# Performance work log

Measured on AMD Instinct MI355X. Metric: run time of the kernel, lower is better.

The kernel has to match this reference:

```python
import jax, jax.numpy as jnp
import numpy as np

N_NODES = 100_000
N_EDGES = 1_600_000
HIDDEN = 256
N_LAYERS = 5
N_GRAPHS = 256
NUM_ATOM_TYPE = 120
NUM_CHIRALITY = 3
NUM_BOND_TYPE = 6
NUM_BOND_DIR = 3


def setup_inputs() -> dict:
    key = jax.random.key(0)
    ks = jax.random.split(key, 16)
    x = jax.random.randint(ks[0], (N_NODES, 2), 0, 3)
    edge_index = jax.random.randint(ks[1], (2, N_EDGES), 0, N_NODES)
    edge_attr = jax.random.randint(ks[2], (N_EDGES, 2), 0, 3)
    batch = jnp.sort(jax.random.randint(ks[3], (N_NODES,), 0, N_GRAPHS))
    # embedding tables (xavier-uniform-ish scale)
    def emb(k, n, d):
        a = np.sqrt(6.0 / (n + d))
        return jax.random.uniform(k, (n, d), jnp.float32, -a, a)
    xe1 = emb(ks[4], NUM_ATOM_TYPE, HIDDEN)
    xe2 = emb(ks[5], NUM_CHIRALITY, HIDDEN)
    ee1 = emb(ks[6], NUM_BOND_TYPE, HIDDEN)
    ee2 = emb(ks[7], NUM_BOND_DIR, HIDDEN)
    s = 1.0 / np.sqrt(HIDDEN)
    W1 = jax.random.uniform(ks[8], (N_LAYERS, HIDDEN, HIDDEN), jnp.float32, -s, s)
    b1 = jax.random.uniform(ks[9], (N_LAYERS, HIDDEN), jnp.float32, -s, s)
    W2 = jax.random.uniform(ks[10], (N_LAYERS, HIDDEN, HIDDEN), jnp.float32, -s, s)
    b2 = jax.random.uniform(ks[11], (N_LAYERS, HIDDEN), jnp.float32, -s, s)
    return {"x": x, "edge_index": edge_index, "edge_attr": edge_attr, "batch": batch,
            "xe1": xe1, "xe2": xe2, "ee1": ee1, "ee2": ee2,
            "W1": W1, "b1": b1, "W2": W2, "b2": b2}


def reference(x, edge_index, edge_attr, batch, xe1, xe2, ee1, ee2, W1, b1, W2, b2):
    # node / edge input embeddings (sum of two lookups)
    z = xe1[x[:, 0]] + xe2[x[:, 1]]                      # [N, H]
    e = ee1[edge_attr[:, 0]] + ee2[edge_attr[:, 1]]      # [E, H]
    src, dst = edge_index[0], edge_index[1]
    for l in range(N_LAYERS):
        # GINEConv: nn((1+eps)*x_i + sum_j relu(x_j + e_ij)), eps = 0
        msg = jax.nn.relu(z[src] + e)                    # [E, H]
        agg = jax.ops.segment_sum(msg, dst, num_segments=N_NODES)
        h = z + agg                                      # (1+0)*x + aggr
        h = jax.nn.relu(h @ W1[l] + b1[l]) @ W2[l] + b2[l]
        z = jax.nn.relu(h)                               # outer relu in GIN.forward
    # global mean pool over graphs
    sums = jax.ops.segment_sum(z, batch, num_segments=N_GRAPHS)      # [G, H]
    cnts = jax.ops.segment_sum(jnp.ones((z.shape[0], 1), z.dtype), batch, num_segments=N_GRAPHS)
    g = sums / jnp.maximum(cnts, 1.0)
    # dropout p=0.0 -> identity
    return (z, g)
```

## Files before the change

kernel.cpp:

```cpp
#include <hip/hip_runtime.h>
#include <hip/hip_bf16.h>

#define HID 256
#define NCODES 18
#define SCAN_CHUNK 2048
#define LROW 264

typedef _Float16 h8_t __attribute__((ext_vector_type(8)));
typedef _Float16 h4_t __attribute__((ext_vector_type(4)));
typedef float f4_t __attribute__((ext_vector_type(4)));

__global__ void etab_kernel(const float* __restrict__ ee1, const float* __restrict__ ee2,
                            _Float16* __restrict__ etab) {
    int t = blockIdx.x;
    int c = threadIdx.x;
    etab[t * HID + c] = (_Float16)(ee1[(t / 3) * HID + c] + ee2[(t % 3) * HID + c]);
}

__global__ __launch_bounds__(256) void embed_kernel(const int* __restrict__ x,
                                                    const float* __restrict__ xe1,
                                                    const float* __restrict__ xe2,
                                                    _Float16* __restrict__ zh, int N) {
    int node = blockIdx.x * 4 + (threadIdx.x >> 6);
    int lane = threadIdx.x & 63;
    if (node >= N) return;
    int a0 = x[node * 2 + 0];
    int a1 = x[node * 2 + 1];
    const float4 u = *(const float4*)(xe1 + (size_t)a0 * HID + lane * 4);
    const float4 v = *(const float4*)(xe2 + (size_t)a1 * HID + lane * 4);
    h4_t r;
    r.x = (_Float16)(u.x + v.x); r.y = (_Float16)(u.y + v.y);
    r.z = (_Float16)(u.z + v.z); r.w = (_Float16)(u.w + v.w);
    *(h4_t*)(zh + (size_t)node * HID + lane * 4) = r;
}

__global__ __launch_bounds__(256) void prep_w(const float* __restrict__ W,
                                              _Float16* __restrict__ Wt) {
    __shared__ float t[32][33];
    int m = blockIdx.z;
    int tx = threadIdx.x & 31, ty = threadIdx.x >> 5;
    const float* Wm = W + (size_t)m * HID * HID;
    _Float16* Wtm = Wt + (size_t)m * HID * HID;
    int k0 = blockIdx.x * 32, n0 = blockIdx.y * 32;
#pragma unroll
    for (int j = 0; j < 4; ++j) { int r = ty + j * 8; t[r][tx] = Wm[(k0 + r) * HID + n0 + tx]; }
    __syncthreads();
#pragma unroll
    for (int j = 0; j < 4; ++j) { int r = ty + j * 8; Wtm[(size_t)(n0 + r) * HID + k0 + tx] = (_Float16)t[tx][r]; }
}

__global__ void hist_kernel(const int* __restrict__ ei, int E, int* __restrict__ deg) {
    int i = blockIdx.x * 256 + threadIdx.x;
    if (i < E) atomicAdd(&deg[ei[E + i]], 1);
}

__global__ __launch_bounds__(256) void scan_partial(const int* __restrict__ deg, int n,
                                                    int* __restrict__ psum) {
    __shared__ int red[256];
    int base = blockIdx.x * SCAN_CHUNK;
    int s = 0;
    for (int i = threadIdx.x; i < SCAN_CHUNK; i += 256) {
        int idx = base + i;
        if (idx < n) s += deg[idx];
    }
    red[threadIdx.x] = s;
    __syncthreads();
    for (int off = 128; off > 0; off >>= 1) {
        if (threadIdx.x < off) red[threadIdx.x] += red[threadIdx.x + off];
        __syncthreads();
    }
    if (threadIdx.x == 0) psum[blockIdx.x] = red[0];
}

__global__ void scan_sums(int* psum, int nchunks) {
    if (blockIdx.x == 0 && threadIdx.x == 0) {
        int acc = 0;
        for (int i = 0; i < nchunks; i++) { int v = psum[i]; psum[i] = acc; acc += v; }
    }
}

__global__ __launch_bounds__(256) void scan_apply(const int* __restrict__ deg, int n,
                                                  const int* __restrict__ psum,
                                                  int* __restrict__ row_start,
                                                  int* __restrict__ cursor, int E) {
    __shared__ int tmp[256];
    int tid = threadIdx.x;
    int base = blockIdx.x * SCAN_CHUNK;
    int tb = base + tid * 8;
    int loc[8];
    int s = 0;
    for (int j = 0; j < 8; j++) {
        loc[j] = s;
        int idx = tb + j;
        if (idx < n) s += deg[idx];
    }
    tmp[tid] = s;
    __syncthreads();
    for (int off = 1; off < 256; off <<= 1) {
        int v = 0;
        if (tid >= off) v = tmp[tid - off];
        __syncthreads();
        if (tid >= off) tmp[tid] += v;
        __syncthreads();
    }
    int excl = tmp[tid] - s + psum[blockIdx.x];
    for (int j = 0; j < 8; j++) {
        int idx = tb + j;
        if (idx < n) {
            int v = excl + loc[j];
            row_start[idx] = v;
            cursor[idx] = v;
        }
    }
    if (blockIdx.x == 0 && tid == 0) row_start[n] = E;
}

__global__ void fill_kernel(const int* __restrict__ ei, const int* __restrict__ ea, int E,
                            int* __restrict__ cursor, unsigned* __restrict__ csr) {
    int i = blockIdx.x * 256 + threadIdx.x;
    if (i >= E) return;
    int dst = ei[E + i];
    int src = ei[i];
    int code = ea[i * 2] * 3 + ea[i * 2 + 1];
    int p = atomicAdd(&cursor[dst], 1);
    csr[p] = (unsigned)src | ((unsigned)code << 20);
}

__global__ __launch_bounds__(256) void agg_kernel(const _Float16* __restrict__ zh,
                                                  const int* __restrict__ row_start,
                                                  const unsigned* __restrict__ csr,
                                                  const _Float16* __restrict__ etab,
                                                  _Float16* __restrict__ h0h, int N) {
    int tid = threadIdx.x;
    int node = blockIdx.x * 8 + (tid >> 5);
    int l32 = tid & 31;
    if (node >= N) return;
    h8_t self = *(const h8_t*)(zh + (size_t)node * HID + l32 * 8);
    float acc[8];
#pragma unroll
    for (int j = 0; j < 8; ++j) acc[j] = (float)self[j];
    int s = row_start[node];
    int e = row_start[node + 1];
    int i = s;
    for (; i + 2 <= e; i += 2) {
        unsigned p0 = csr[i], p1 = csr[i + 1];
        h8_t z0 = *(const h8_t*)(zh + (size_t)(p0 & 0xFFFFF) * HID + l32 * 8);
        h8_t e0 = *(const h8_t*)(etab + (size_t)(p0 >> 20) * HID + l32 * 8);
        h8_t z1 = *(const h8_t*)(zh + (size_t)(p1 & 0xFFFFF) * HID + l32 * 8);
        h8_t e1 = *(const h8_t*)(etab + (size_t)(p1 >> 20) * HID + l32 * 8);
#pragma unroll
        for (int j = 0; j < 8; ++j) {
            acc[j] += fmaxf((float)z0[j] + (float)e0[j], 0.f);
            acc[j] += fmaxf((float)z1[j] + (float)e1[j], 0.f);
        }
    }
    if (i < e) {
        unsigned p0 = csr[i];
        h8_t z0 = *(const h8_t*)(zh + (size_t)(p0 & 0xFFFFF) * HID + l32 * 8);
        h8_t e0 = *(const h8_t*)(etab + (size_t)(p0 >> 20) * HID + l32 * 8);
#pragma unroll
        for (int j = 0; j < 8; ++j) acc[j] += fmaxf((float)z0[j] + (float)e0[j], 0.f);
    }
    h8_t o;
#pragma unroll
    for (int j = 0; j < 8; ++j) o[j] = (_Float16)acc[j];
    *(h8_t*)(h0h + (size_t)node * HID + l32 * 8) = o;
}

__global__ __launch_bounds__(256, 2) void mlp_fused(const _Float16* __restrict__ A,
                                                    const _Float16* __restrict__ Wt1,
                                                    const float* __restrict__ b1,
                                                    const _Float16* __restrict__ Wt2,
                                                    const float* __restrict__ b2,
                                                    _Float16* __restrict__ outh,
                                                    float* __restrict__ outf,
                                                    int M, int writef) {
    __shared__ _Float16 As[64 * LROW];
    __shared__ _Float16 Ys[64 * LROW];
    int tid = threadIdx.x;
    int lane = tid & 63;
    int w = tid >> 6;
    int row0 = blockIdx.x * 64;
    const _Float16* Ab = A + (size_t)row0 * HID;

#pragma unroll
    for (int it = 0; it < 8; ++it) {
        int c = it * 256 + tid;
        int row = c >> 5, cir = c & 31;
        h8_t v = *(const h8_t*)(Ab + row * HID + cir * 8);
        *(h8_t*)(As + row * LROW + cir * 8) = v;
    }
    __syncthreads();

    int wc = w * 64;
    int l16 = lane & 15;
    int lq = lane >> 4;

    {
        f4_t acc[4][4] = {};
#pragma unroll
        for (int ks = 0; ks < 8; ++ks) {
            h8_t a[4], b[4];
#pragma unroll
            for (int mi = 0; mi < 4; ++mi)
                a[mi] = *(const h8_t*)(As + (mi * 16 + l16) * LROW + (ks * 4 + lq) * 8);
#pragma unroll
            for (int ni = 0; ni < 4; ++ni)
                b[ni] = *(const h8_t*)(Wt1 + (size_t)(wc + ni * 16 + l16) * HID + ks * 32 + lq * 8);
#pragma unroll
            for (int mi = 0; mi < 4; ++mi)
#pragma unroll
                for (int ni = 0; ni < 4; ++ni)
                    acc[mi][ni] = __builtin_amdgcn_mfma_f32_16x16x32_f16(a[mi], b[ni], acc[mi][ni], 0, 0, 0);
        }
#pragma unroll
        for (int ni = 0; ni < 4; ++ni) {
            int col = wc + ni * 16 + l16;
            float bv = b1[col];
#pragma unroll
            for (int mi = 0; mi < 4; ++mi)
#pragma unroll
                for (int r = 0; r < 4; ++r) {
                    int rr = mi * 16 + lq * 4 + r;
                    Ys[rr * LROW + col] = (_Float16)fmaxf(acc[mi][ni][r] + bv, 0.f);
                }
        }
    }
    __syncthreads();

    {
        f4_t acc[4][4] = {};
#pragma unroll
        for (int ks = 0; ks < 8; ++ks) {
            h8_t a[4], b[4];
#pragma unroll
            for (int mi = 0; mi < 4; ++mi)
                a[mi] = *(const h8_t*)(Ys + (mi * 16 + l16) * LROW + (ks * 4 + lq) * 8);
#pragma unroll
            for (int ni = 0; ni < 4; ++ni)
                b[ni] = *(const h8_t*)(Wt2 + (size_t)(wc + ni * 16 + l16) * HID + ks * 32 + lq * 8);
#pragma unroll
            for (int mi = 0; mi < 4; ++mi)
#pragma unroll
                for (int ni = 0; ni < 4; ++ni)
                    acc[mi][ni] = __builtin_amdgcn_mfma_f32_16x16x32_f16(a[mi], b[ni], acc[mi][ni], 0, 0, 0);
        }
#pragma unroll
        for (int ni = 0; ni < 4; ++ni) {
            int col = wc + ni * 16 + l16;
            float bv = b2[col];
#pragma unroll
            for (int mi = 0; mi < 4; ++mi)
#pragma unroll
                for (int r = 0; r < 4; ++r) {
                    int rr = mi * 16 + lq * 4 + r;
                    As[rr * LROW + col] = (_Float16)fmaxf(acc[mi][ni][r] + bv, 0.f);
                }
        }
    }
    __syncthreads();

#pragma unroll
    for (int it = 0; it < 8; ++it) {
        int c = it * 256 + tid;
        int row = c >> 5, cir = c & 31;
        int grow = row0 + row;
        if (grow < M) {
            h8_t v = *(const h8_t*)(As + row * LROW + cir * 8);
            *(h8_t*)(outh + (size_t)grow * HID + cir * 8) = v;
            if (writef) {
                f4_t f0, f1;
#pragma unroll
                for (int j = 0; j < 4; ++j) { f0[j] = (float)v[j]; f1[j] = (float)v[j + 4]; }
                *(f4_t*)(outf + (size_t)grow * HID + cir * 8) = f0;
                *(f4_t*)(outf + (size_t)grow * HID + cir * 8 + 4) = f1;
            }
        }
    }
}

__global__ __launch_bounds__(1024) void pool_kernel(const _Float16* __restrict__ zh,
                                                    const int* __restrict__ batch, int N,
                                                    float* __restrict__ g) {
    __shared__ float red[32 * 32 * 8];
    int gid = blockIdx.x;
    int lo = 0, hi = N;
    while (lo < hi) { int mid = (lo + hi) >> 1; if (batch[mid] < gid) lo = mid + 1; else hi = mid; }
    int start = lo;
    int lo2 = start, hi2 = N;
    while (lo2 < hi2) { int mid = (lo2 + hi2) >> 1; if (batch[mid] < gid + 1) lo2 = mid + 1; else hi2 = mid; }
    int end = lo2;
    int cnt = end - start;

    int r = threadIdx.x >> 5;
    int ch = threadIdx.x & 31;
    float acc[8] = {};
    for (int row = start + r; row < end; row += 32) {
        h8_t v = *(const h8_t*)(zh + (size_t)row * HID + ch * 8);
#pragma unroll
        for (int j = 0; j < 8; ++j) acc[j] += (float)v[j];
    }
    float* slot = red + (r * 32 + ch) * 8;
#pragma unroll
    for (int j = 0; j < 8; ++j) slot[j] = acc[j];
    __syncthreads();
    for (int off = 16; off > 0; off >>= 1) {
        if (r < off) {
            const float* o = red + ((r + off) * 32 + ch) * 8;
#pragma unroll
            for (int j = 0; j < 8; ++j) { acc[j] += o[j]; slot[j] = acc[j]; }
        }
        __syncthreads();
    }
    if (r == 0) {
        float inv = 1.0f / fmaxf((float)cnt, 1.0f);
#pragma unroll
        for (int j = 0; j < 8; ++j) g[(size_t)gid * HID + ch * 8 + j] = acc[j] * inv;
    }
}

extern "C" void kernel_launch(void* const* d_in, const int* in_sizes, int n_in,
                              void* d_out, int out_size, void* d_ws, size_t ws_size,
                              hipStream_t stream) {
    const int* x = (const int*)d_in[0];
    const int* ei = (const int*)d_in[1];
    const int* ea = (const int*)d_in[2];
    const int* batch = (const int*)d_in[3];
    const float* xe1 = (const float*)d_in[4];
    const float* xe2 = (const float*)d_in[5];
    const float* ee1 = (const float*)d_in[6];
    const float* ee2 = (const float*)d_in[7];
    const float* W1 = (const float*)d_in[8];
    const float* b1 = (const float*)d_in[9];
    const float* W2 = (const float*)d_in[10];
    const float* b2 = (const float*)d_in[11];

    int N = in_sizes[0] / 2;
    int E = in_sizes[1] / 2;
    int G = out_size / HID - N;
    int Np = ((N + 127) / 128) * 128;
    int nbm = (N + 63) / 64;

    float* z = (float*)d_out;
    float* gout = z + (size_t)N * HID;

    char* w = (char*)d_ws;
    _Float16* h0h = (_Float16*)w;  w += (size_t)Np * HID * 2;
    _Float16* zh  = (_Float16*)w;  w += (size_t)Np * HID * 2;
    _Float16* Wt1 = (_Float16*)w;  w += (size_t)5 * HID * HID * 2;
    _Float16* Wt2 = (_Float16*)w;  w += (size_t)5 * HID * HID * 2;
    _Float16* etabh = (_Float16*)w; w += (size_t)NCODES * HID * 2;
    int* deg = (int*)w;       w += (size_t)N * 4;
    int* row_start = (int*)w; w += (size_t)(N + 1) * 4;
    int* cursor = (int*)w;    w += (size_t)N * 4;
    int* psum = (int*)w;      w += 64 * 4;
    unsigned* csr = (unsigned*)w;

    hipMemsetAsync(deg, 0, (size_t)N * 4, stream);
    etab_kernel<<<NCODES, HID, 0, stream>>>(ee1, ee2, etabh);
    embed_kernel<<<(N + 3) / 4, 256, 0, stream>>>(x, xe1, xe2, zh, N);
    prep_w<<<dim3(8, 8, 5), 256, 0, stream>>>(W1, Wt1);
    prep_w<<<dim3(8, 8, 5), 256, 0, stream>>>(W2, Wt2);
    hist_kernel<<<(E + 255) / 256, 256, 0, stream>>>(ei, E, deg);
    int nchunks = (N + SCAN_CHUNK - 1) / SCAN_CHUNK;
    scan_partial<<<nchunks, 256, 0, stream>>>(deg, N, psum);
    scan_sums<<<1, 1, 0, stream>>>(psum, nchunks);
    scan_apply<<<nchunks, 256, 0, stream>>>(deg, N, psum, row_start, cursor, E);
    fill_kernel<<<(E + 255) / 256, 256, 0, stream>>>(ei, ea, E, cursor, csr);

    for (int l = 0; l < 5; l++) {
        agg_kernel<<<(N + 7) / 8, 256, 0, stream>>>(zh, row_start, csr, etabh, h0h, N);
        mlp_fused<<<nbm, 256, 0, stream>>>(h0h, Wt1 + (size_t)l * HID * HID,
                                           b1 + (size_t)l * HID,
                                           Wt2 + (size_t)l * HID * HID,
                                           b2 + (size_t)l * HID,
                                           zh, z, N, (l == 4) ? 1 : 0);
    }
    pool_kernel<<<G, 1024, 0, stream>>>(zh, batch, N, gout);
}
```

Before: 1.280 ms.

## Fuse edge aggregation into per-layer MLP kernel with ping-pong node buffers

Merges the separate aggregation kernel into the fused MLP kernel. Each 64-row block now gathers neighbour features and edge embeddings directly into shared memory before running the two GEMMs. This removes the round trip of the intermediate h0 buffer through global memory and one launch per layer. Two node buffers alternate between layers because a layer can no longer write its output in place while other blocks still read it. The message add and ReLU now run in packed fp16 and the inner loop is unrolled by four. The cost is that the gather phase runs at the MLP kernel's low occupancy (two 256-thread blocks per CU, limited by shared memory), so there is less latency hiding for the random gathers, plus some loss of precision.

```diff
diff --git a/kernel.cpp b/kernel.cpp
--- a/kernel.cpp
+++ b/kernel.cpp
@@ -126,69 +126,71 @@
     csr[p] = (unsigned)src | ((unsigned)code << 20);
 }
 
-__global__ __launch_bounds__(256) void agg_kernel(const _Float16* __restrict__ zh,
-                                                  const int* __restrict__ row_start,
-                                                  const unsigned* __restrict__ csr,
-                                                  const _Float16* __restrict__ etab,
-                                                  _Float16* __restrict__ h0h, int N) {
-    int tid = threadIdx.x;
-    int node = blockIdx.x * 8 + (tid >> 5);
-    int l32 = tid & 31;
-    if (node >= N) return;
-    h8_t self = *(const h8_t*)(zh + (size_t)node * HID + l32 * 8);
-    float acc[8];
-#pragma unroll
-    for (int j = 0; j < 8; ++j) acc[j] = (float)self[j];
-    int s = row_start[node];
-    int e = row_start[node + 1];
-    int i = s;
-    for (; i + 2 <= e; i += 2) {
-        unsigned p0 = csr[i], p1 = csr[i + 1];
-        h8_t z0 = *(const h8_t*)(zh + (size_t)(p0 & 0xFFFFF) * HID + l32 * 8);
-        h8_t e0 = *(const h8_t*)(etab + (size_t)(p0 >> 20) * HID + l32 * 8);
-        h8_t z1 = *(const h8_t*)(zh + (size_t)(p1 & 0xFFFFF) * HID + l32 * 8);
-        h8_t e1 = *(const h8_t*)(etab + (size_t)(p1 >> 20) * HID + l32 * 8);
-#pragma unroll
-        for (int j = 0; j < 8; ++j) {
-            acc[j] += fmaxf((float)z0[j] + (float)e0[j], 0.f);
-            acc[j] += fmaxf((float)z1[j] + (float)e1[j], 0.f);
-        }
-    }
-    if (i < e) {
-        unsigned p0 = csr[i];
-        h8_t z0 = *(const h8_t*)(zh + (size_t)(p0 & 0xFFFFF) * HID + l32 * 8);
-        h8_t e0 = *(const h8_t*)(etab + (size_t)(p0 >> 20) * HID + l32 * 8);
-#pragma unroll
-        for (int j = 0; j < 8; ++j) acc[j] += fmaxf((float)z0[j] + (float)e0[j], 0.f);
-    }
-    h8_t o;
-#pragma unroll
-    for (int j = 0; j < 8; ++j) o[j] = (_Float16)acc[j];
-    *(h8_t*)(h0h + (size_t)node * HID + l32 * 8) = o;
-}
-
-__global__ __launch_bounds__(256, 2) void mlp_fused(const _Float16* __restrict__ A,
-                                                    const _Float16* __restrict__ Wt1,
-                                                    const float* __restrict__ b1,
-                                                    const _Float16* __restrict__ Wt2,
-                                                    const float* __restrict__ b2,
-                                                    _Float16* __restrict__ outh,
-                                                    float* __restrict__ outf,
-                                                    int M, int writef) {
+__global__ __launch_bounds__(256, 2) void layer_fused(const _Float16* __restrict__ zin,
+                                                      const int* __restrict__ row_start,
+                                                      const unsigned* __restrict__ csr,
+                                                      const _Float16* __restrict__ etab,
+                                                      const _Float16* __restrict__ Wt1,
+                                                      const float* __restrict__ b1,
+                                                      const _Float16* __restrict__ Wt2,
+                                                      const float* __restrict__ b2,
+                                                      _Float16* __restrict__ zout,
+                                                      float* __restrict__ outf,
+                                                      int M, int writef) {
     __shared__ _Float16 As[64 * LROW];
     __shared__ _Float16 Ys[64 * LROW];
     int tid = threadIdx.x;
     int lane = tid & 63;
     int w = tid >> 6;
     int row0 = blockIdx.x * 64;
-    const _Float16* Ab = A + (size_t)row0 * HID;
-
-#pragma unroll
-    for (int it = 0; it < 8; ++it) {
-        int c = it * 256 + tid;
-        int row = c >> 5, cir = c & 31;
-        h8_t v = *(const h8_t*)(Ab + row * HID + cir * 8);
-        *(h8_t*)(As + row * LROW + cir * 8) = v;
+
+    {
+        int l32 = tid & 31;
+        int half = (tid >> 5) & 1;
+        const h8_t hz = {};
+        for (int t = 0; t < 8; ++t) {
+            int row = w * 16 + t * 2 + half;
+            int node = row0 + row;
+            float acc[8] = {};
+            if (node < M) {
+                h8_t self = *(const h8_t*)(zin + (size_t)node * HID + l32 * 8);
+#pragma unroll
+                for (int j = 0; j < 8; ++j) acc[j] = (float)self[j];
+                int s = row_start[node];
+                int e = row_start[node + 1];
+                int i = s;
+                for (; i + 4 <= e; i += 4) {
+                    unsigned p0 = csr[i], p1 = csr[i + 1], p2 = csr[i + 2], p3 = csr[i + 3];
+                    h8_t z0 = *(const h8_t*)(zin + (size_t)(p0 & 0xFFFFF) * HID + l32 * 8);
+                    h8_t z1 = *(const h8_t*)(zin + (size_t)(p1 & 0xFFFFF) * HID + l32 * 8);
+                    h8_t z2 = *(const h8_t*)(zin + (size_t)(p2 & 0xFFFFF) * HID + l32 * 8);
+                    h8_t z3 = *(const h8_t*)(zin + (size_t)(p3 & 0xFFFFF) * HID + l32 * 8);
+                    h8_t e0 = *(const h8_t*)(etab + (size_t)(p0 >> 20) * HID + l32 * 8);
+                    h8_t e1 = *(const h8_t*)(etab + (size_t)(p1 >> 20) * HID + l32 * 8);
+                    h8_t e2 = *(const h8_t*)(etab + (size_t)(p2 >> 20) * HID + l32 * 8);
+                    h8_t e3 = *(const h8_t*)(etab + (size_t)(p3 >> 20) * HID + l32 * 8);
+                    h8_t m0 = __builtin_elementwise_max(z0 + e0, hz);
+                    h8_t m1 = __builtin_elementwise_max(z1 + e1, hz);
+                    h8_t m2 = __builtin_elementwise_max(z2 + e2, hz);
+                    h8_t m3 = __builtin_elementwise_max(z3 + e3, hz);
+#pragma unroll
+                    for (int j = 0; j < 8; ++j)
+                        acc[j] += (float)m0[j] + (float)m1[j] + (float)m2[j] + (float)m3[j];
+                }
+                for (; i < e; ++i) {
+                    unsigned p0 = csr[i];
+                    h8_t z0 = *(const h8_t*)(zin + (size_t)(p0 & 0xFFFFF) * HID + l32 * 8);
+                    h8_t e0 = *(const h8_t*)(etab + (size_t)(p0 >> 20) * HID + l32 * 8);
+                    h8_t m0 = __builtin_elementwise_max(z0 + e0, hz);
+#pragma unroll
+                    for (int j = 0; j < 8; ++j) acc[j] += (float)m0[j];
+                }
+            }
+            h8_t o;
+#pragma unroll
+            for (int j = 0; j < 8; ++j) o[j] = (_Float16)acc[j];
+            *(h8_t*)(As + row * LROW + l32 * 8) = o;
+        }
     }
     __syncthreads();
 
@@ -267,7 +269,7 @@
         int grow = row0 + row;
         if (grow < M) {
             h8_t v = *(const h8_t*)(As + row * LROW + cir * 8);
-            *(h8_t*)(outh + (size_t)grow * HID + cir * 8) = v;
+            *(h8_t*)(zout + (size_t)grow * HID + cir * 8) = v;
             if (writef) {
                 f4_t f0, f1;
 #pragma unroll
@@ -338,15 +340,15 @@
     int N = in_sizes[0] / 2;
     int E = in_sizes[1] / 2;
     int G = out_size / HID - N;
-    int Np = ((N + 127) / 128) * 128;
     int nbm = (N + 63) / 64;
+    int Np = nbm * 64;
 
     float* z = (float*)d_out;
     float* gout = z + (size_t)N * HID;
 
     char* w = (char*)d_ws;
-    _Float16* h0h = (_Float16*)w;  w += (size_t)Np * HID * 2;
-    _Float16* zh  = (_Float16*)w;  w += (size_t)Np * HID * 2;
+    _Float16* zhA = (_Float16*)w;  w += (size_t)Np * HID * 2;
+    _Float16* zhB = (_Float16*)w;  w += (size_t)Np * HID * 2;
     _Float16* Wt1 = (_Float16*)w;  w += (size_t)5 * HID * HID * 2;
     _Float16* Wt2 = (_Float16*)w;  w += (size_t)5 * HID * HID * 2;
     _Float16* etabh = (_Float16*)w; w += (size_t)NCODES * HID * 2;
@@ -358,7 +360,7 @@
 
     hipMemsetAsync(deg, 0, (size_t)N * 4, stream);
     etab_kernel<<<NCODES, HID, 0, stream>>>(ee1, ee2, etabh);
-    embed_kernel<<<(N + 3) / 4, 256, 0, stream>>>(x, xe1, xe2, zh, N);
+    embed_kernel<<<(N + 3) / 4, 256, 0, stream>>>(x, xe1, xe2, zhA, N);
     prep_w<<<dim3(8, 8, 5), 256, 0, stream>>>(W1, Wt1);
     prep_w<<<dim3(8, 8, 5), 256, 0, stream>>>(W2, Wt2);
     hist_kernel<<<(E + 255) / 256, 256, 0, stream>>>(ei, E, deg);
@@ -369,12 +371,12 @@
     fill_kernel<<<(E + 255) / 256, 256, 0, stream>>>(ei, ea, E, cursor, csr);
 
     for (int l = 0; l < 5; l++) {
-        agg_kernel<<<(N + 7) / 8, 256, 0, stream>>>(zh, row_start, csr, etabh, h0h, N);
-        mlp_fused<<<nbm, 256, 0, stream>>>(h0h, Wt1 + (size_t)l * HID * HID,
-                                           b1 + (size_t)l * HID,
-                                           Wt2 + (size_t)l * HID * HID,
-                                           b2 + (size_t)l * HID,
-                                           zh, z, N, (l == 4) ? 1 : 0);
-    }
-    pool_kernel<<<G, 1024, 0, stream>>>(zh, batch, N, gout);
-}
+        const _Float16* zin = (l & 1) ? zhB : zhA;
+        _Float16* zout = (l & 1) ? zhA : zhB;
+        layer_fused<<<nbm, 256, 0, stream>>>(zin, row_start, csr, etabh,
+                                             Wt1 + (size_t)l * HID * HID, b1 + (size_t)l * HID,
+                                             Wt2 + (size_t)l * HID * HID, b2 + (size_t)l * HID,
+                                             zout, z, N, (l == 4) ? 1 : 0);
+    }
+    pool_kernel<<<G, 1024, 0, stream>>>(zhB, batch, N, gout);
+}
```

New measurement: 1.548 ms. 21.0% more time.
